# Kernel tuning notes

Measured on AMD Instinct MI355X. Metric: run time of the kernel, lower is better.

The kernel has to match this reference:

```python
import jax, jax.numpy as jnp
import numpy as np

TEMP = 1.0
EPS = 1e-6


def trop_linear(x, w, b, temp=TEMP):
    # x: (..., in), w: (out, in) -> (..., out)
    # y_i = temp * logsumexp_j((w_ij + x_j)/temp) + b_i  (soft tropical / max-plus)
    z = x[..., None, :] + w  # (..., out, in)
    y = temp * jax.nn.logsumexp(z / temp, axis=-1)
    return y + b


def trop_layernorm(x, weight, bias, eps=EPS):
    n = x.shape[-1]
    # torch.median returns the lower of the two middle elements for even n
    med = jnp.sort(x, axis=-1)[..., (n - 1) // 2][..., None]
    q75 = jnp.quantile(x, 0.75, axis=-1, keepdims=True)
    q25 = jnp.quantile(x, 0.25, axis=-1, keepdims=True)
    iqr = jnp.maximum(q75 - q25, eps)
    return (x - med) / iqr * weight + bias


def setup_inputs() -> dict:
    key = jax.random.key(0)
    ks = jax.random.split(key, 8)
    B, D_IN, D_H, D_OUT = 1024, 512, 512, 256
    return {
        "x": jax.random.normal(ks[0], (B, D_IN), dtype=jnp.float32),
        "w1": 0.1 * jax.random.normal(ks[1], (D_H, D_IN), dtype=jnp.float32),
        "b1": jnp.zeros((D_H,), dtype=jnp.float32),
        "ln1_w": jnp.ones((D_H,), dtype=jnp.float32),
        "ln1_b": jnp.zeros((D_H,), dtype=jnp.float32),
        "w2": 0.1 * jax.random.normal(ks[2], (D_H, D_H), dtype=jnp.float32),
        "b2": jnp.zeros((D_H,), dtype=jnp.float32),
        "ln2_w": jnp.ones((D_H,), dtype=jnp.float32),
        "ln2_b": jnp.zeros((D_H,), dtype=jnp.float32),
        "w3": 0.1 * jax.random.normal(ks[3], (D_OUT, D_H), dtype=jnp.float32),
        "b3": jnp.zeros((D_OUT,), dtype=jnp.float32),
    }


def reference(x, w1, b1, ln1_w, ln1_b, w2, b2, ln2_w, ln2_b, w3, b3):
    h = trop_linear(x, w1, b1)
    h = trop_layernorm(h, ln1_w, ln1_b)
    h = jnp.maximum(h, 0.0)  # TropicalActivation('relu', threshold=0)
    h = trop_linear(h, w2, b2)
    h = trop_layernorm(h, ln2_w, ln2_b)
    h = jnp.maximum(h, 0.0)
    return trop_linear(h, w3, b3)
```

## Files before the change

### kernel.cpp

```cpp
#include <hip/hip_runtime.h>
#include <math.h>


typedef float v4f __attribute__((ext_vector_type(4)));

#define ELS_B 528
#define LN64f 4.1588830833596715f

__device__ __forceinline__ int pk4_fp8(float a, float b, float c, float d) {
    int p = __builtin_amdgcn_cvt_pk_fp8_f32(a, b, 0, 0);
    p = __builtin_amdgcn_cvt_pk_fp8_f32(c, d, p, 1);
    return p;
}

__global__ __launch_bounds__(256) void expW_frag(const float* __restrict__ w1,
                                                 const float* __restrict__ w2,
                                                 const float* __restrict__ w3,
                                                 uint8_t* __restrict__ Ef) {
    int u = blockIdx.x * 256 + threadIdx.x;
    int lane = u & 63, t = (u >> 6) & 15, S = u >> 10;
    int r = lane & 15, q = lane >> 4;
    const float* w; int tile;
    if (S < 32)      { w = w1; tile = S; }
    else if (S < 64) { w = w2; tile = S - 32; }
    else             { w = w3; tile = S - 64; }
    const float* src = w + (tile * 16 + r) * 512 + t * 32 + q * 8;
    float4 a = *reinterpret_cast<const float4*>(src);
    float4 b = *reinterpret_cast<const float4*>(src + 4);
    int2 o;
    o.x = pk4_fp8(__expf(a.x), __expf(a.y), __expf(a.z), __expf(a.w));
    o.y = pk4_fp8(__expf(b.x), __expf(b.y), __expf(b.z), __expf(b.w));
    *reinterpret_cast<int2*>(Ef + u * 8) = o;
}

__device__ __forceinline__ void load_areg(const uint8_t* Els, int lane, long* areg) {
    const uint8_t* ap = Els + (lane & 3) * ELS_B + ((lane >> 4) & 3) * 8;
#pragma unroll
    for (int t = 0; t < 16; ++t)
        areg[t] = *reinterpret_cast<const long*>(ap + t * 32);
}

template <int NSUB>
__device__ __forceinline__ void gemm_frag(const uint8_t* __restrict__ Bf,
                                          int s0, int lane,
                                          const long* areg, v4f* acc) {
    const uint8_t* bp = Bf + lane * 8;
    long bb[8][NSUB];
#pragma unroll
    for (int p = 0; p < 8; ++p)
#pragma unroll
        for (int s = 0; s < NSUB; ++s)
            bb[p][s] = *reinterpret_cast<const long*>(bp + ((s0 + s) * 16 + p) * 512);
#pragma unroll
    for (int s = 0; s < NSUB; ++s) acc[s] = (v4f){0.f, 0.f, 0.f, 0.f};
#pragma unroll
    for (int t = 0; t < 16; ++t) {
        long a = areg[t];
        long bcur[NSUB];
#pragma unroll
        for (int s = 0; s < NSUB; ++s) bcur[s] = bb[t & 7][s];
        if (t < 8) {
#pragma unroll
            for (int s = 0; s < NSUB; ++s)
                bb[t & 7][s] =
                    *reinterpret_cast<const long*>(bp + ((s0 + s) * 16 + t + 8) * 512);
        }
#pragma unroll
        for (int s = 0; s < NSUB; ++s)
            acc[s] = __builtin_amdgcn_mfma_f32_16x16x32_fp8_fp8(a, bcur[s],
                                                                acc[s], 0, 0, 0);
    }
}

__device__ __forceinline__ void ln_row(const float* hbuf,
                                       const float* __restrict__ lw,
                                       const float* __restrict__ lb,
                                       uint8_t* Els, float* crow,
                                       int w, int lane) {
    float h[8], v[8];
    {
        const float* hp = hbuf + w * 512 + lane * 8;
        float4 a = *reinterpret_cast<const float4*>(hp);
        float4 b = *reinterpret_cast<const float4*>(hp + 4);
        h[0] = a.x; h[1] = a.y; h[2] = a.z; h[3] = a.w;
        h[4] = b.x; h[5] = b.y; h[6] = b.z; h[7] = b.w;
#pragma unroll
        for (int j = 0; j < 8; ++j) v[j] = h[j];
    }
#pragma unroll
    for (int k = 2; k <= 512; k <<= 1) {
#pragma unroll
        for (int jj = 256; jj > 0; jj >>= 1) {
            if (jj >= k) continue;
            if (jj >= 8) {
                int lm = jj >> 3;
#pragma unroll
                for (int j = 0; j < 8; ++j) {
                    float pv = __shfl_xor(v[j], lm);
                    bool up = ((((lane << 3) | j) & k) == 0);
                    bool low = ((lane & lm) == 0);
                    v[j] = (up == low) ? fminf(v[j], pv) : fmaxf(v[j], pv);
                }
            } else {
#pragma unroll
                for (int j = 0; j < 8; ++j) {
                    if (j & jj) continue;
                    int jh = j | jj;
                    bool up = ((((lane << 3) | j) & k) == 0);
                    float a = v[j], c = v[jh];
                    float lo = fminf(a, c), hi = fmaxf(a, c);
                    v[j] = up ? lo : hi;
                    v[jh] = up ? hi : lo;
                }
            }
        }
    }
    float s127 = __shfl(v[7], 15);
    float s128 = __shfl(v[0], 16);
    float med  = __shfl(v[7], 31);
    float s383 = __shfl(v[7], 47);
    float s384 = __shfl(v[0], 48);
    float q25 = s127 + 0.75f * (s128 - s127);
    float q75 = s383 + 0.25f * (s384 - s383);
    float inv = 1.0f / fmaxf(q75 - q25, 1e-6f);

    float y[8], cm = 0.0f;
    {
        const float4* lw4 = reinterpret_cast<const float4*>(lw + lane * 8);
        const float4* lb4 = reinterpret_cast<const float4*>(lb + lane * 8);
        float4 wa = lw4[0], wb = lw4[1], ba = lb4[0], bbv = lb4[1];
        float lwv[8] = {wa.x, wa.y, wa.z, wa.w, wb.x, wb.y, wb.z, wb.w};
        float lbv[8] = {ba.x, ba.y, ba.z, ba.w, bbv.x, bbv.y, bbv.z, bbv.w};
#pragma unroll
        for (int j = 0; j < 8; ++j) {
            y[j] = fmaxf((h[j] - med) * inv * lwv[j] + lbv[j], 0.0f);
            cm = fmaxf(cm, y[j]);
        }
    }
#pragma unroll
    for (int s = 32; s > 0; s >>= 1) cm = fmaxf(cm, __shfl_xor(cm, s));
    {
        float e[8];
#pragma unroll
        for (int j = 0; j < 8; ++j) e[j] = 64.0f * __expf(y[j] - cm);
        int2 o;
        o.x = pk4_fp8(e[0], e[1], e[2], e[3]);
        o.y = pk4_fp8(e[4], e[5], e[6], e[7]);
        *reinterpret_cast<int2*>(&Els[w * ELS_B + lane * 8]) = o;
    }
    if (lane == 0) crow[w] = cm;
}

__global__ __launch_bounds__(512, 2) void fused_rows(
    const float* __restrict__ x,
    const float* __restrict__ b1,
    const float* __restrict__ ln1w, const float* __restrict__ ln1b,
    const float* __restrict__ b2,
    const float* __restrict__ ln2w, const float* __restrict__ ln2b,
    const float* __restrict__ b3,
    const uint8_t* __restrict__ Ew,
    float* __restrict__ out)
{
    __shared__ uint8_t Els[4 * ELS_B];
    __shared__ float hbuf[4 * 512];
    __shared__ float crow[4];

    const int tid = threadIdx.x;
    const int lane = tid & 63;
    const int w = tid >> 6;
    const int r = lane & 15, q = lane >> 4;
    const int blk = blockIdx.x;

    {
        int row = tid >> 7, col = (tid & 127) * 4;
        float4 a = *reinterpret_cast<const float4*>(x + blk * 2048 + row * 512 + col);
        *reinterpret_cast<int*>(&Els[row * ELS_B + col]) =
            pk4_fp8(4.0f * __expf(a.x), 4.0f * __expf(a.y),
                    4.0f * __expf(a.z), 4.0f * __expf(a.w));
    }
    __syncthreads();

    long areg[16];
    v4f acc[4];

    load_areg(Els, lane, areg);
    gemm_frag<4>(Ew, w * 4, lane, areg, acc);
    if (q == 0) {
#pragma unroll
        for (int s = 0; s < 4; ++s) {
            int col = (w * 4 + s) * 16 + r;
            float bb = b1[col];
#pragma unroll
            for (int t = 0; t < 4; ++t)
                hbuf[t * 512 + col] = __logf(acc[s][t]) + bb;
        }
    }
    __syncthreads();
    if (w < 4) ln_row(hbuf, ln1w, ln1b, Els, crow, w, lane);
    __syncthreads();

    load_areg(Els, lane, areg);
    gemm_frag<4>(Ew + 262144, w * 4, lane, areg, acc);
    if (q == 0) {
#pragma unroll
        for (int s = 0; s < 4; ++s) {
            int col = (w * 4 + s) * 16 + r;
            float bb = b2[col];
#pragma unroll
            for (int t = 0; t < 4; ++t)
                hbuf[t * 512 + col] = __logf(acc[s][t]) + bb;
        }
    }
    __syncthreads();
    if (w < 4) ln_row(hbuf, ln2w, ln2b, Els, crow, w, lane);
    __syncthreads();

    load_areg(Els, lane, areg);
    gemm_frag<2>(Ew + 524288, w * 2, lane, areg, acc);
    if (q == 0) {
#pragma unroll
        for (int s = 0; s < 2; ++s) {
            int col = (w * 2 + s) * 16 + r;
            float bb = b3[col] - LN64f;
#pragma unroll
            for (int t = 0; t < 4; ++t)
                out[(blk * 4 + t) * 256 + col] = __logf(acc[s][t]) + crow[t] + bb;
        }
    }
}

extern "C" void kernel_launch(void* const* d_in, const int* in_sizes, int n_in,
                              void* d_out, int out_size, void* d_ws, size_t ws_size,
                              hipStream_t stream) {
    const float* x    = (const float*)d_in[0];
    const float* w1   = (const float*)d_in[1];
    const float* b1   = (const float*)d_in[2];
    const float* ln1w = (const float*)d_in[3];
    const float* ln1b = (const float*)d_in[4];
    const float* w2   = (const float*)d_in[5];
    const float* b2   = (const float*)d_in[6];
    const float* ln2w = (const float*)d_in[7];
    const float* ln2b = (const float*)d_in[8];
    const float* w3   = (const float*)d_in[9];
    const float* b3   = (const float*)d_in[10];
    float* out = (float*)d_out;

    uint8_t* Ew = (uint8_t*)d_ws;

    expW_frag<<<320, 256, 0, stream>>>(w1, w2, w3, Ew);
    fused_rows<<<256, 512, 0, stream>>>(x, b1, ln1w, ln1b, b2, ln2w, ln2b,
                                        b3, Ew, out);
}
```

Measured before the change: 97.99 us.

## Prefetch next layer's weight fragments before barriers to overlap with layernorm

Splits the fragment GEMM into a prefetch step and a compute step. The first eight B-fragment loads of each layer are issued early: before the input exp/pack for layer 1, and before the barrier and layernorm for layers 2 and 3. The layernorm weight and bias loads are also hoisted to the top of ln_row. The aim is to hide global-memory latency behind the sort and layernorm work, at the cost of keeping 32 longs of B registers live across the layernorm, which raises register pressure.

```diff
diff --git a/kernel.cpp b/kernel.cpp
--- a/kernel.cpp
+++ b/kernel.cpp
@@ -41,16 +41,19 @@
 }
 
 template <int NSUB>
-__device__ __forceinline__ void gemm_frag(const uint8_t* __restrict__ Bf,
-                                          int s0, int lane,
-                                          const long* areg, v4f* acc) {
-    const uint8_t* bp = Bf + lane * 8;
-    long bb[8][NSUB];
+__device__ __forceinline__ void prefetchB(const uint8_t* __restrict__ bp,
+                                          int s0, long bb[8][4]) {
 #pragma unroll
     for (int p = 0; p < 8; ++p)
 #pragma unroll
         for (int s = 0; s < NSUB; ++s)
             bb[p][s] = *reinterpret_cast<const long*>(bp + ((s0 + s) * 16 + p) * 512);
+}
+
+template <int NSUB>
+__device__ __forceinline__ void gemm_body(const uint8_t* __restrict__ bp,
+                                          int s0, const long* areg,
+                                          long bb[8][4], v4f* acc) {
 #pragma unroll
     for (int s = 0; s < NSUB; ++s) acc[s] = (v4f){0.f, 0.f, 0.f, 0.f};
 #pragma unroll
@@ -77,6 +80,10 @@
                                        const float* __restrict__ lb,
                                        uint8_t* Els, float* crow,
                                        int w, int lane) {
+    const float4* lw4 = reinterpret_cast<const float4*>(lw + lane * 8);
+    const float4* lb4 = reinterpret_cast<const float4*>(lb + lane * 8);
+    float4 wa = lw4[0], wb = lw4[1], ba = lb4[0], bbv = lb4[1];
+
     float h[8], v[8];
     {
         const float* hp = hbuf + w * 512 + lane * 8;
@@ -126,9 +133,6 @@
 
     float y[8], cm = 0.0f;
     {
-        const float4* lw4 = reinterpret_cast<const float4*>(lw + lane * 8);
-        const float4* lb4 = reinterpret_cast<const float4*>(lb + lane * 8);
-        float4 wa = lw4[0], wb = lw4[1], ba = lb4[0], bbv = lb4[1];
         float lwv[8] = {wa.x, wa.y, wa.z, wa.w, wb.x, wb.y, wb.z, wb.w};
         float lbv[8] = {ba.x, ba.y, ba.z, ba.w, bbv.x, bbv.y, bbv.z, bbv.w};
 #pragma unroll
@@ -171,6 +175,16 @@
     const int r = lane & 15, q = lane >> 4;
     const int blk = blockIdx.x;
 
+    const uint8_t* bp1 = Ew + lane * 8;
+    const uint8_t* bp2 = bp1 + 262144;
+    const uint8_t* bp3 = bp1 + 524288;
+
+    long bb[8][4];
+    long areg[16];
+    v4f acc[4];
+
+    prefetchB<4>(bp1, w * 4, bb);
+
     {
         int row = tid >> 7, col = (tid & 127) * 4;
         float4 a = *reinterpret_cast<const float4*>(x + blk * 2048 + row * 512 + col);
@@ -180,51 +194,50 @@
     }
     __syncthreads();
 
-    long areg[16];
-    v4f acc[4];
-
     load_areg(Els, lane, areg);
-    gemm_frag<4>(Ew, w * 4, lane, areg, acc);
+    gemm_body<4>(bp1, w * 4, areg, bb, acc);
     if (q == 0) {
 #pragma unroll
         for (int s = 0; s < 4; ++s) {
             int col = (w * 4 + s) * 16 + r;
-            float bb = b1[col];
+            float bbv = b1[col];
 #pragma unroll
             for (int t = 0; t < 4; ++t)
-                hbuf[t * 512 + col] = __logf(acc[s][t]) + bb;
-        }
-    }
+                hbuf[t * 512 + col] = __logf(acc[s][t]) + bbv;
+        }
+    }
+    prefetchB<4>(bp2, w * 4, bb);
     __syncthreads();
     if (w < 4) ln_row(hbuf, ln1w, ln1b, Els, crow, w, lane);
     __syncthreads();
 
     load_areg(Els, lane, areg);
-    gemm_frag<4>(Ew + 262144, w * 4, lane, areg, acc);
+    gemm_body<4>(bp2, w * 4, areg, bb, acc);
     if (q == 0) {
 #pragma unroll
         for (int s = 0; s < 4; ++s) {
             int col = (w * 4 + s) * 16 + r;
-            float bb = b2[col];
+            float bbv = b2[col];
 #pragma unroll
             for (int t = 0; t < 4; ++t)
-                hbuf[t * 512 + col] = __logf(acc[s][t]) + bb;
-        }
-    }
+                hbuf[t * 512 + col] = __logf(acc[s][t]) + bbv;
+        }
+    }
+    prefetchB<2>(bp3, w * 2, bb);
     __syncthreads();
     if (w < 4) ln_row(hbuf, ln2w, ln2b, Els, crow, w, lane);
     __syncthreads();
 
     load_areg(Els, lane, areg);
-    gemm_frag<2>(Ew + 524288, w * 2, lane, areg, acc);
+    gemm_body<2>(bp3, w * 2, areg, bb, acc);
     if (q == 0) {
 #pragma unroll
         for (int s = 0; s < 2; ++s) {
             int col = (w * 2 + s) * 16 + r;
-            float bb = b3[col] - LN64f;
+            float bbv = b3[col] - LN64f;
 #pragma unroll
             for (int t = 0; t < 4; ++t)
-                out[(blk * 4 + t) * 256 + col] = __logf(acc[s][t]) + crow[t] + bb;
+                out[(blk * 4 + t) * 256 + col] = __logf(acc[s][t]) + crow[t] + bbv;
         }
     }
 }
```

Result: faster. 94.88 us (-3.2%).
